# Kernel tuning notes

Hardware: AMD Instinct MI355X
Metric: run time of the kernel (lower is better)

The kernel has to match this reference:

```python
import jax, jax.numpy as jnp
import numpy as np

LAYERS = [3, 1024, 512, 256, 128, 1]
WIDTHS = [3, 1024, 1024, 1024, 1024, 1]  # width per BsPINN: 2^(i-1)*Layers[i]
N = 131072


def _mask(num_blocks, bs1, bs2):
    # block-diagonal mask of ones, built statically (constant under jit)
    return jnp.asarray(np.kron(np.eye(num_blocks, dtype=np.float32),
                               np.ones((bs1, bs2), dtype=np.float32)))


def _xavier(key, shape, fan_in, fan_out):
    lim = np.sqrt(6.0 / (fan_in + fan_out)).astype(np.float32)
    return jax.random.uniform(key, shape, jnp.float32, -lim, lim)


def setup_inputs() -> dict:
    key = jax.random.key(0)
    ks = jax.random.split(key, 6)
    inp = {
        "X": jax.random.uniform(ks[0], (N, 3), dtype=jnp.float32),
        "lb_X": jnp.zeros((3,), jnp.float32),
        "ub_X": jnp.ones((3,), jnp.float32),
    }
    for i in range(5):
        # xavier scale per sub-block Layers[i] x Layers[i+1], as in the torch init
        inp[f"W{i}"] = _xavier(ks[i + 1], (WIDTHS[i], WIDTHS[i + 1]),
                               LAYERS[i], LAYERS[i + 1])
        inp[f"b{i}"] = jnp.zeros((1, WIDTHS[i + 1]), jnp.float32)
    return inp


def reference(X, lb_X, ub_X, W0, b0, W1, b1, W2, b2, W3, b3, W4, b4):
    # masks for hidden layers l=2,3: 2 blocks of 512x512, 4 blocks of 256x256
    m2 = _mask(2, LAYERS[2], 2 * LAYERS[3])   # [1024,1024]
    m3 = _mask(4, LAYERS[3], 2 * LAYERS[4])   # [1024,1024]
    h = 2.0 * (X - lb_X) / (ub_X - lb_X) - 1.0  # [N,3]
    h = jnp.sin(h @ W0 + b0)            # [N,1024] dense
    h = jnp.sin(h @ W1 + b1)            # [N,1024] dense
    h = jnp.sin(h @ (W2 * m2) + b2)     # [N,1024] block-diag (2 blocks)
    h = jnp.sin(h @ (W3 * m3) + b3)     # [N,1024] block-diag (4 blocks)
    return h @ W4 + b4                  # [N,1]
```

## Files before the change

### kernel.cpp

```cpp
#include <hip/hip_runtime.h>

typedef _Float16 f16x8 __attribute__((ext_vector_type(8)));
typedef _Float16 f16x4 __attribute__((ext_vector_type(4)));
typedef float f32x4 __attribute__((ext_vector_type(4)));
typedef unsigned int u32;

#define ROWS 64
#define THREADS 512

__global__ __launch_bounds__(512) void pack_weights(
    const float* __restrict__ W1, const float* __restrict__ W2,
    const float* __restrict__ W3, _Float16* __restrict__ WF1,
    _Float16* __restrict__ WF2, _Float16* __restrict__ WF3) {
  int t = blockIdx.x * 512 + threadIdx.x;
  const float* src; _Float16* dst; int idx, ct, kt, lane, kbase;
  if (t < 131072) {
    idx = t; src = W1; dst = WF1;
    ct = idx >> 11; kt = (idx >> 6) & 31; lane = idx & 63; kbase = 0;
  } else if (t < 196608) {
    idx = t - 131072; src = W2; dst = WF2;
    ct = idx >> 10; kt = (idx >> 6) & 15; lane = idx & 63;
    kbase = (ct >= 32) ? 512 : 0;
  } else {
    idx = t - 196608; src = W3; dst = WF3;
    ct = idx >> 9; kt = (idx >> 6) & 7; lane = idx & 63;
    kbase = (ct >> 4) << 8;
  }
  int c  = ct * 16 + (lane & 15);
  int k0 = kbase + kt * 32 + ((lane >> 4) << 3);
  f16x8 v;
#pragma unroll
  for (int j = 0; j < 8; ++j) v[j] = (_Float16)src[(size_t)(k0 + j) * 1024 + c];
  *reinterpret_cast<f16x8*>(dst + (size_t)idx * 8) = v;
}

template <int KT>
__device__ __forceinline__ void layer_mfma(char* hb, const _Float16* __restrict__ WF,
                                           const float* __restrict__ bias,
                                           int wid, int lane, int kbase) {
  f32x4 acc[8][4];
#pragma unroll
  for (int cf = 0; cf < 8; ++cf)
#pragma unroll
    for (int rf = 0; rf < 4; ++rf) acc[cf][rf] = f32x4{0.f, 0.f, 0.f, 0.f};

  const f16x8* wf = reinterpret_cast<const f16x8*>(WF) +
                    (u32)(wid * 8 * KT * 64 + lane);
  const int arow = lane & 15;
  const int koff = (lane >> 4) << 3;
  const u32 abase = (u32)(arow * 2048);
  const u32 axor  = (u32)((arow & 7) << 4);

  f16x8 wA[8], wB[8];
#define LOADW(buf, ktv)                                                        \
  { u32 _kt = (u32)(ktv);                                                      \
    _Pragma("unroll") for (int cf = 0; cf < 8; ++cf)                           \
      buf[cf] = wf[(u32)(cf * KT) * 64u + _kt * 64u]; }
#define DOMFMA(buf, ktv)                                                       \
  { int _kt = (ktv);                                                           \
    u32 kb = (u32)((kbase + _kt * 32 + koff) * 2);                             \
    f16x8 h[4];                                                                \
    _Pragma("unroll") for (int rf = 0; rf < 4; ++rf) {                         \
      u32 addr = ((u32)(rf * 32768) + abase + kb) ^ axor;                      \
      h[rf] = *reinterpret_cast<const f16x8*>(hb + addr);                      \
    }                                                                          \
    _Pragma("unroll") for (int cf = 0; cf < 8; ++cf)                           \
      _Pragma("unroll") for (int rf = 0; rf < 4; ++rf)                         \
        acc[cf][rf] = __builtin_amdgcn_mfma_f32_16x16x32_f16(buf[cf], h[rf],   \
                                                             acc[cf][rf], 0, 0, 0); }

  LOADW(wA, 0);
#pragma unroll 1
  for (int kt = 0; kt < KT; kt += 2) {
    LOADW(wB, kt + 1);
    DOMFMA(wA, kt);
    LOADW(wA, (kt + 2 < KT) ? (kt + 2) : 0);
    DOMFMA(wB, kt + 1);
  }
#undef LOADW
#undef DOMFMA

  __syncthreads();
  const int csub = (lane >> 4) << 2;
  const int rr   = lane & 15;
#pragma unroll
  for (int cf = 0; cf < 8; ++cf) {
    int c0 = wid * 128 + cf * 16 + csub;
    f32x4 bb = *reinterpret_cast<const f32x4*>(bias + c0);
#pragma unroll
    for (int rf = 0; rf < 4; ++rf) {
      int r = rf * 16 + rr;
      f16x4 pk;
#pragma unroll
      for (int i = 0; i < 4; ++i) pk[i] = (_Float16)__sinf(acc[cf][rf][i] + bb[i]);
      u32 addr = ((u32)(r * 2048 + c0 * 2)) ^ ((u32)((r & 7) << 4));
      *reinterpret_cast<f16x4*>(hb + addr) = pk;
    }
  }
  __syncthreads();
}

__global__
__attribute__((amdgpu_flat_work_group_size(512, 512), amdgpu_waves_per_eu(2, 2)))
void bspinn_fused(
    const float* __restrict__ X, const float* __restrict__ lb,
    const float* __restrict__ ub,
    const float* __restrict__ W0, const float* __restrict__ b0,
    const _Float16* __restrict__ WF1, const float* __restrict__ b1,
    const _Float16* __restrict__ WF2, const float* __restrict__ b2,
    const _Float16* __restrict__ WF3, const float* __restrict__ b3,
    const float* __restrict__ W4, const float* __restrict__ b4,
    float* __restrict__ out) {
  __shared__ alignas(16) char hb[ROWS * 2048];
  __shared__ float xs[ROWS * 4];
  __shared__ float partials[ROWS * 8];

  const int tid  = threadIdx.x;
  const int lane = tid & 63;
  const int wid  = tid >> 6;
  const int r0   = blockIdx.x * ROWS;

  if (tid < ROWS * 3) {
    int r = tid / 3, j = tid - r * 3;
    float x = X[(size_t)r0 * 3 + tid];
    xs[r * 4 + j] = 2.0f * (x - lb[j]) / (ub[j] - lb[j]) - 1.0f;
  }
  __syncthreads();

  {
    int c0 = tid * 2;
    float wa0 = W0[c0],        wb0 = W0[c0 + 1];
    float wa1 = W0[1024 + c0], wb1 = W0[1025 + c0];
    float wa2 = W0[2048 + c0], wb2 = W0[2049 + c0];
    float ba = b0[c0], bbv = b0[c0 + 1];
#pragma unroll 4
    for (int r = 0; r < ROWS; ++r) {
      float x0 = xs[r * 4], x1 = xs[r * 4 + 1], x2 = xs[r * 4 + 2];
      float va = __sinf(fmaf(x2, wa2, fmaf(x1, wa1, fmaf(x0, wa0, ba))));
      float vb = __sinf(fmaf(x2, wb2, fmaf(x1, wb1, fmaf(x0, wb0, bbv))));
      union { _Float16 h2[2]; u32 u; } pk;
      pk.h2[0] = (_Float16)va; pk.h2[1] = (_Float16)vb;
      u32 addr = ((u32)(r * 2048 + c0 * 2)) ^ ((u32)((r & 7) << 4));
      *reinterpret_cast<u32*>(hb + addr) = pk.u;
    }
  }
  __syncthreads();

  layer_mfma<32>(hb, WF1, b1, wid, lane, 0);
  layer_mfma<16>(hb, WF2, b2, wid, lane, (wid >> 2) * 512);
  layer_mfma<8 >(hb, WF3, b3, wid, lane, (wid >> 1) * 256);

  {
    int r = lane, seg = wid;
    u32 rb = (u32)(r * 2048);
    u32 xr = (u32)((r & 7) << 4);
    float s = 0.f;
#pragma unroll
    for (int kk = 0; kk < 128; kk += 8) {
      int k = seg * 128 + kk;
      f16x8 v = *reinterpret_cast<const f16x8*>(hb + ((rb + (u32)(k * 2)) ^ xr));
#pragma unroll
      for (int j = 0; j < 8; ++j) s = fmaf((float)v[j], W4[k + j], s);
    }
    partials[seg * 64 + r] = s;
  }
  __syncthreads();
  if (tid < ROWS) {
    float s = b4[0];
#pragma unroll
    for (int g = 0; g < 8; ++g) s += partials[g * 64 + tid];
    out[r0 + tid] = s;
  }
}

extern "C" void kernel_launch(void* const* d_in, const int* in_sizes, int n_in,
                              void* d_out, int out_size, void* d_ws, size_t ws_size,
                              hipStream_t stream) {
  const float* X  = (const float*)d_in[0];
  const float* lb = (const float*)d_in[1];
  const float* ub = (const float*)d_in[2];
  const float* W0 = (const float*)d_in[3];
  const float* b0 = (const float*)d_in[4];
  const float* W1 = (const float*)d_in[5];
  const float* b1 = (const float*)d_in[6];
  const float* W2 = (const float*)d_in[7];
  const float* b2 = (const float*)d_in[8];
  const float* W3 = (const float*)d_in[9];
  const float* b3 = (const float*)d_in[10];
  const float* W4 = (const float*)d_in[11];
  const float* b4 = (const float*)d_in[12];
  float* out = (float*)d_out;

  _Float16* WF1 = (_Float16*)d_ws;
  _Float16* WF2 = (_Float16*)((char*)d_ws + 2097152);
  _Float16* WF3 = (_Float16*)((char*)d_ws + 2097152 + 1048576);

  hipLaunchKernelGGL(pack_weights, dim3(448), dim3(512), 0, stream,
                     W1, W2, W3, WF1, WF2, WF3);
  hipLaunchKernelGGL(bspinn_fused, dim3(131072 / ROWS), dim3(THREADS), 0, stream,
                     X, lb, ub, W0, b0, WF1, b1, WF2, b2, WF3, b3, W4, b4, out);
}
```

Before: 521.1 us.

## Double-buffer LDS activation loads, raise MFMA priority, use packed f16 conversion

Activation fragments are now loaded from LDS one k-step ahead into double buffers (hA/hB), alongside the existing weight prefetch, so LDS latency can overlap with MFMA work. MFMA blocks are wrapped in s_setprio to favour matrix issue across waves. The f32-to-f16 conversions switch to packed round-toward-zero cvt_pkrtz, which cuts conversion instructions but changes rounding slightly. The extra buffers raise VGPR pressure, which could cause spills at the fixed two waves per EU.

After: 491.4 us. 1.06x faster.

```diff
diff --git a/kernel.cpp b/kernel.cpp
--- a/kernel.cpp
+++ b/kernel.cpp
@@ -2,6 +2,7 @@
 
 typedef _Float16 f16x8 __attribute__((ext_vector_type(8)));
 typedef _Float16 f16x4 __attribute__((ext_vector_type(4)));
+typedef __fp16  fp16x2 __attribute__((ext_vector_type(2)));
 typedef float f32x4 __attribute__((ext_vector_type(4)));
 typedef unsigned int u32;
 
@@ -51,33 +52,39 @@
   const u32 abase = (u32)(arow * 2048);
   const u32 axor  = (u32)((arow & 7) << 4);
 
-  f16x8 wA[8], wB[8];
+  f16x8 wA[8], wB[8], hA[4], hB[4];
 #define LOADW(buf, ktv)                                                        \
   { u32 _kt = (u32)(ktv);                                                      \
     _Pragma("unroll") for (int cf = 0; cf < 8; ++cf)                           \
       buf[cf] = wf[(u32)(cf * KT) * 64u + _kt * 64u]; }
-#define DOMFMA(buf, ktv)                                                       \
-  { int _kt = (ktv);                                                           \
-    u32 kb = (u32)((kbase + _kt * 32 + koff) * 2);                             \
-    f16x8 h[4];                                                                \
+#define LDH(buf, ktv)                                                          \
+  { u32 kb = (u32)((kbase + (ktv) * 32 + koff) * 2);                           \
     _Pragma("unroll") for (int rf = 0; rf < 4; ++rf) {                         \
       u32 addr = ((u32)(rf * 32768) + abase + kb) ^ axor;                      \
-      h[rf] = *reinterpret_cast<const f16x8*>(hb + addr);                      \
-    }                                                                          \
+      buf[rf] = *reinterpret_cast<const f16x8*>(hb + addr);                    \
+    } }
+#define DOMFMA(w, h)                                                           \
+  { __builtin_amdgcn_s_setprio(1);                                             \
     _Pragma("unroll") for (int cf = 0; cf < 8; ++cf)                           \
       _Pragma("unroll") for (int rf = 0; rf < 4; ++rf)                         \
-        acc[cf][rf] = __builtin_amdgcn_mfma_f32_16x16x32_f16(buf[cf], h[rf],   \
-                                                             acc[cf][rf], 0, 0, 0); }
+        acc[cf][rf] = __builtin_amdgcn_mfma_f32_16x16x32_f16(w[cf], h[rf],     \
+                                                             acc[cf][rf], 0, 0, 0); \
+    __builtin_amdgcn_s_setprio(0); }
 
   LOADW(wA, 0);
+  LDH(hA, 0);
 #pragma unroll 1
   for (int kt = 0; kt < KT; kt += 2) {
+    int ktn = (kt + 2 < KT) ? (kt + 2) : 0;
     LOADW(wB, kt + 1);
-    DOMFMA(wA, kt);
-    LOADW(wA, (kt + 2 < KT) ? (kt + 2) : 0);
-    DOMFMA(wB, kt + 1);
+    LDH(hB, kt + 1);
+    DOMFMA(wA, hA);
+    LOADW(wA, ktn);
+    LDH(hA, ktn);
+    DOMFMA(wB, hB);
   }
 #undef LOADW
+#undef LDH
 #undef DOMFMA
 
   __syncthreads();
@@ -90,11 +97,15 @@
 #pragma unroll
     for (int rf = 0; rf < 4; ++rf) {
       int r = rf * 16 + rr;
-      f16x4 pk;
-#pragma unroll
-      for (int i = 0; i < 4; ++i) pk[i] = (_Float16)__sinf(acc[cf][rf][i] + bb[i]);
+      float s0 = __sinf(acc[cf][rf][0] + bb[0]);
+      float s1 = __sinf(acc[cf][rf][1] + bb[1]);
+      float s2 = __sinf(acc[cf][rf][2] + bb[2]);
+      float s3 = __sinf(acc[cf][rf][3] + bb[3]);
+      union { fp16x2 h2[2]; f16x4 v; } pk;
+      pk.h2[0] = __builtin_amdgcn_cvt_pkrtz(s0, s1);
+      pk.h2[1] = __builtin_amdgcn_cvt_pkrtz(s2, s3);
       u32 addr = ((u32)(r * 2048 + c0 * 2)) ^ ((u32)((r & 7) << 4));
-      *reinterpret_cast<f16x4*>(hb + addr) = pk;
+      *reinterpret_cast<f16x4*>(hb + addr) = pk.v;
     }
   }
   __syncthreads();
@@ -138,8 +149,8 @@
       float x0 = xs[r * 4], x1 = xs[r * 4 + 1], x2 = xs[r * 4 + 2];
       float va = __sinf(fmaf(x2, wa2, fmaf(x1, wa1, fmaf(x0, wa0, ba))));
       float vb = __sinf(fmaf(x2, wb2, fmaf(x1, wb1, fmaf(x0, wb0, bbv))));
-      union { _Float16 h2[2]; u32 u; } pk;
-      pk.h2[0] = (_Float16)va; pk.h2[1] = (_Float16)vb;
+      union { fp16x2 h2; u32 u; } pk;
+      pk.h2 = __builtin_amdgcn_cvt_pkrtz(va, vb);
       u32 addr = ((u32)(r * 2048 + c0 * 2)) ^ ((u32)((r & 7) << 4));
       *reinterpret_cast<u32*>(hb + addr) = pk.u;
     }
```
